# Performance work log

Hardware: AMD Instinct MI355X
Metric: run time of the kernel (lower is better)

The kernel has to match this reference:

```python
import jax, jax.numpy as jnp
import numpy as np
import math

B, S, D_MODEL, HEADS, GRID = 4, 2048, 512, 8, 8
HEAD_DIM = D_MODEL // HEADS
A_C, K_C, C_C = 0.9724108095811765, 0.9884401790754128, 0.999449553483052


def setup_inputs() -> dict:
    key = jax.random.key(0)
    ks = jax.random.split(key, 4)
    q = jax.random.normal(ks[0], (B, S, D_MODEL), jnp.float32)
    mask = jnp.tril(jnp.ones((S, S), dtype=bool))[None, None]  # causal (1,1,S,S)
    out_dim = 3 * D_MODEL
    grid_norm = jnp.arange(1, GRID + 1, dtype=jnp.float32)  # (grid,)
    # is_first=True init: normal(0,0.4)/output_dim/grid_norm_factor
    amplitudes = jax.random.normal(ks[1], (out_dim, D_MODEL, GRID), jnp.float32) * 0.4 / out_dim / grid_norm
    # norm_freq with is_first=True -> freq = arange(1..grid) / (grid+1)**0 = arange
    freq = jnp.arange(1, GRID + 1, dtype=jnp.float32)  # (grid,)
    grid_phase = jnp.arange(1, GRID + 1, dtype=jnp.float32) / (GRID + 1)
    input_phase = jnp.linspace(0.0, math.pi, D_MODEL, dtype=jnp.float32)[:, None]  # (in,1)
    phase0 = grid_phase[None, :] + input_phase  # (in, grid)
    ratio = 1.0
    for i in range(1, GRID):
        ratio *= A_C * i ** (-K_C) + C_C
    phase = phase0 * np.float32(ratio)
    kan_bias = jnp.ones((out_dim,), jnp.float32) / out_dim
    lim = math.sqrt(6.0 / (D_MODEL + D_MODEL))  # xavier_uniform
    out_w = jax.random.uniform(ks[2], (D_MODEL, D_MODEL), jnp.float32, -lim, lim)
    out_b = jnp.zeros((D_MODEL,), jnp.float32)
    return {"q": q, "mask": mask, "freq": freq, "phase": phase,
            "amplitudes": amplitudes, "kan_bias": kan_bias,
            "out_w": out_w, "out_b": out_b}


def sinekan(x2d, freq, phase, amp, bias):
    # y[n,j] = sum_{k,l} sin(x[n,k]*f[l] + p[k,l]) * amp[j,k,l] + bias[j]
    # expand sin(a+p) = sin(a)cos(p) + cos(a)sin(p); fold phase into weights
    ang = x2d[:, :, None] * freq  # (N, in, grid)
    w_sin = amp * jnp.cos(phase)  # (out, in, grid)
    w_cos = amp * jnp.sin(phase)
    y = (jnp.einsum('nkl,jkl->nj', jnp.sin(ang), w_sin)
         + jnp.einsum('nkl,jkl->nj', jnp.cos(ang), w_cos))
    return y + bias


def rotate_half(u):
    u1, u2 = jnp.split(u, 2, axis=-1)
    return jnp.concatenate([-u2, u1], axis=-1)


def apply_rope(x, pos_emb):
    cos, sin = jnp.split(pos_emb, 2, axis=-1)  # each (S, head_dim//2)
    x_even, x_odd = x[..., ::2], x[..., 1::2]
    x1 = x_even * cos + rotate_half(x_odd) * sin
    x2 = x_odd * cos + rotate_half(x_even) * sin
    return jnp.concatenate([x1, x2], axis=-1)


def rope_emb(seq_len, dim):
    half = dim // 2
    inv_freq = 1.0 / (10000.0 ** (jnp.arange(half, dtype=jnp.float32) / half))
    ang = jnp.arange(seq_len, dtype=jnp.float32)[:, None] * inv_freq  # (S, half)
    return jnp.concatenate([jnp.cos(ang), jnp.sin(ang)], axis=-1)  # (S, dim)


def reference(q, mask, freq, phase, amplitudes, kan_bias, out_w, out_b):
    b, s, _ = q.shape
    qkv = sinekan(q.reshape(-1, D_MODEL), freq, phase, amplitudes, kan_bias)
    qkv = qkv.reshape(b, s, HEADS, 3 * HEAD_DIM).transpose(0, 2, 1, 3)  # (b,h,s,3d)
    qs, ks, vs = jnp.split(qkv, 3, axis=-1)
    pe = rope_emb(s, HEAD_DIM)
    qs = apply_rope(qs, pe)
    ks = apply_rope(ks, pe)
    scores = jnp.einsum('bhqd,bhkd->bhqk', qs, ks) / math.sqrt(HEAD_DIM)
    scores = jnp.where(mask, scores.astype(jnp.float32), -1e9)
    attn = jax.nn.softmax(scores, axis=-1)
    ctx = jnp.einsum('bhqk,bhkd->bhqd', attn, vs)
    ctx = ctx.transpose(0, 2, 1, 3).reshape(b, s, D_MODEL)
    return ctx @ out_w.T + out_b
```

## Files before the change

kernel.cpp:

```cpp
#include <hip/hip_runtime.h>
#include <math.h>


typedef __attribute__((ext_vector_type(8))) short bf16x8;
typedef __attribute__((ext_vector_type(8))) unsigned short ushort8;
typedef __attribute__((ext_vector_type(4))) float f32x4;

#define DEV __device__ __forceinline__

DEV unsigned short f2bf(float f) {
  unsigned u = __builtin_bit_cast(unsigned, f);
  u += 0x7FFFu + ((u >> 16) & 1u);
  return (unsigned short)(u >> 16);
}
DEV float bf2f(unsigned short h) {
  unsigned u = ((unsigned)h) << 16;
  return __builtin_bit_cast(float, u);
}

#define GLDS16(gp, lp)                                                         \
  __builtin_amdgcn_global_load_lds(                                            \
      (const __attribute__((address_space(1))) void*)(gp),                     \
      (__attribute__((address_space(3))) void*)(lp), 16, 0, 0)

__global__ __launch_bounds__(256) void wprep(const float* __restrict__ amp,
                                             const float* __restrict__ phase,
                                             unsigned short* __restrict__ Wb) {
  int id = blockIdx.x * 256 + threadIdx.x;
  int j = id >> 9;
  int k = id & 511;
  const float* ap = amp + (size_t)id * 8;
  const float* ph = phase + k * 8;
  union { unsigned short u[16]; uint4 v[2]; } pk;
#pragma unroll
  for (int l = 0; l < 8; ++l) {
    float sp, cp;
    sincosf(ph[l], &sp, &cp);
    float a = ap[l];
    pk.u[l] = f2bf(a * cp);
    pk.u[8 + l] = f2bf(a * sp);
  }
  uint4* dst = (uint4*)(Wb + (size_t)j * 8192 + k * 16);
  dst[0] = pk.v[0];
  dst[1] = pk.v[1];
}

__global__ __launch_bounds__(256) void owprep(const float* __restrict__ w,
                                              unsigned short* __restrict__ o) {
  int id = blockIdx.x * 256 + threadIdx.x;
  o[id] = f2bf(w[id]);
}

__global__ __launch_bounds__(256) void fgen(const float* __restrict__ q,
                                            unsigned short* __restrict__ F) {
  int id = blockIdx.x * 256 + threadIdx.x;
  int row = id >> 9;
  int dim = id & 511;
  float x = q[(size_t)row * 512 + dim];
  float s1, c1;
  sincosf(x, &s1, &c1);
  union { unsigned short u[16]; uint4 v[2]; } fr;
  float s = s1, c = c1;
  fr.u[0] = f2bf(s);
  fr.u[8] = f2bf(c);
#pragma unroll
  for (int l = 1; l < 8; ++l) {
    float ns = s * c1 + c * s1;
    float nc = c * c1 - s * s1;
    s = ns; c = nc;
    fr.u[l] = f2bf(s);
    fr.u[8 + l] = f2bf(c);
  }
  uint4* dst = (uint4*)(F + (size_t)row * 8192 + dim * 16);
  dst[0] = fr.v[0];
  dst[1] = fr.v[1];
}

__global__ __launch_bounds__(512, 2) void kan_gemm8(
    const unsigned short* __restrict__ F, const unsigned short* __restrict__ Wb,
    const float* __restrict__ bias, unsigned short* __restrict__ qkv) {
  __shared__ __align__(16) char LDS[114688];

  const int tid = threadIdx.x, lane = tid & 63, wid = tid >> 6;
  const int wm = wid >> 2, wn = wid & 3;
  const int l15 = lane & 15, kg = lane >> 4;

  int bid = blockIdx.x;
  int xcd = bid & 7, u = bid >> 3;
  const int m0 = (xcd * 4 + (u & 3)) * 256;
  const int n0 = (u >> 2) * 192;

  const int growl = wid * 8 + (lane >> 3);
  const int cswz = ((lane & 7) ^ (lane >> 3)) << 4;

  f32x4 acc[2][4][3] = {};
  bf16x8 af0[4][2], af1[4][2], bf[3][2];

#define STAGE_A(T, C)                                                           \
  GLDS16((const char*)F + (size_t)(m0 + (C)*64 + growl) * 16384 +               \
             (size_t)(T) * 128 + cswz,                                          \
         LDS + (((T)&1) * 32768 + (C)*8192 + wid * 1024))

#define STAGE_B(T, C)                                                           \
  GLDS16((const char*)Wb + (size_t)(n0 + (C)*64 + growl) * 16384 +              \
             (size_t)(T) * 128 + cswz,                                          \
         LDS + (65536 + ((T)&1) * 24576 + (C)*8192 + wid * 1024))

#define DSREAD_A(DST, T, MQ)                                                    \
  do {                                                                          \
    _Pragma("unroll") for (int mi = 0; mi < 4; ++mi)                            \
        _Pragma("unroll") for (int kk = 0; kk < 2; ++kk) {                      \
      int _r = (MQ)*128 + wm * 64 + mi * 16 + l15;                              \
      DST[mi][kk] = *(const bf16x8*)(LDS + ((T)&1) * 32768 + _r * 128 +         \
                                     (((kk * 4 + kg) ^ (l15 & 7)) << 4));       \
    }                                                                           \
  } while (0)

#define DSREAD_B(T)                                                             \
  do {                                                                          \
    _Pragma("unroll") for (int ni = 0; ni < 3; ++ni)                            \
        _Pragma("unroll") for (int kk = 0; kk < 2; ++kk) {                      \
      int _r = wn * 48 + ni * 16 + l15;                                         \
      bf[ni][kk] = *(const bf16x8*)(LDS + 65536 + ((T)&1) * 24576 + _r * 128 +  \
                                    (((kk * 4 + kg) ^ (l15 & 7)) << 4));        \
    }                                                                           \
  } while (0)

#define MFMAS(AF, MQ, NI0, NI1)                                                 \
  do {                                                                          \
    __builtin_amdgcn_s_setprio(1);                                              \
    _Pragma("unroll") for (int mi = 0; mi < 4; ++mi)                            \
        _Pragma("unroll") for (int ni = (NI0); ni <= (NI1); ++ni)               \
            _Pragma("unroll") for (int kk = 0; kk < 2; ++kk)                    \
                acc[MQ][mi][ni] = __builtin_amdgcn_mfma_f32_16x16x32_bf16(      \
                    AF[mi][kk], bf[ni][kk], acc[MQ][mi][ni], 0, 0, 0);          \
    __builtin_amdgcn_s_setprio(0);                                              \
  } while (0)

#define BAR __builtin_amdgcn_s_barrier()
#define VMW(N) asm volatile("s_waitcnt vmcnt(" #N ")" ::: "memory")
#define LGW                                                                     \
  do {                                                                          \
    asm volatile("s_waitcnt lgkmcnt(0)" ::: "memory");                          \
    __builtin_amdgcn_sched_barrier(0);                                          \
  } while (0)

  STAGE_A(0, 0); STAGE_A(0, 1);
  STAGE_B(0, 0); STAGE_B(0, 1); STAGE_B(0, 2);
  STAGE_A(0, 2); STAGE_A(0, 3);

#pragma unroll 2
  for (int t = 0; t < 127; ++t) {
    VMW(2); BAR;
    DSREAD_A(af0, t, 0); DSREAD_B(t);
    STAGE_A(t + 1, 0); STAGE_A(t + 1, 1);
    LGW; MFMAS(af0, 0, 0, 1);
    BAR;
    DSREAD_A(af1, t, 1);
    STAGE_B(t + 1, 0); STAGE_B(t + 1, 1);
    MFMAS(af0, 0, 2, 2);
    VMW(4); BAR;
    STAGE_B(t + 1, 2); STAGE_A(t + 1, 2);
    MFMAS(af1, 1, 0, 1);
    BAR;
    STAGE_A(t + 1, 3);
    MFMAS(af1, 1, 2, 2);
  }
  {
    const int t = 127;
    VMW(2); BAR;
    DSREAD_A(af0, t, 0); DSREAD_B(t);
    LGW; MFMAS(af0, 0, 0, 1);
    BAR;
    DSREAD_A(af1, t, 1);
    MFMAS(af0, 0, 2, 2);
    VMW(0); BAR;
    MFMAS(af1, 1, 0, 1);
    BAR;
    MFMAS(af1, 1, 2, 2);
  }

#pragma unroll
  for (int mq = 0; mq < 2; ++mq)
#pragma unroll
    for (int mi = 0; mi < 4; ++mi)
#pragma unroll
      for (int ni = 0; ni < 3; ++ni) {
        int row = m0 + mq * 128 + wm * 64 + mi * 16 + kg * 4;
        int col = n0 + wn * 48 + ni * 16 + l15;
        float bv = bias[col];
        f32x4 a = acc[mq][mi][ni];
#pragma unroll
        for (int j = 0; j < 4; ++j)
          qkv[(size_t)(row + j) * 1536 + col] = f2bf(a[j] + bv);
      }
#undef STAGE_A
#undef STAGE_B
#undef DSREAD_A
#undef DSREAD_B
#undef MFMAS
#undef BAR
#undef VMW
#undef LGW
}

__global__ __launch_bounds__(256) void rope_prep(const unsigned short* __restrict__ qkv,
                                                 unsigned short* __restrict__ Qr,
                                                 unsigned short* __restrict__ Kr) {
  int id = blockIdx.x * 256 + threadIdx.x;
  int i = id & 31;
  int row = id >> 5;
  int s = row & 2047;
  int bh = row >> 11;
  int b = bh >> 3, h = bh & 7;

  const unsigned short* base = qkv + ((size_t)(b * 2048 + s)) * 1536 + h * 192;

  float inv = exp2f(-(float)i * (13.287712379549449f / 32.0f));
  float ang = (float)s * inv;
  float sn, cs;
  sincosf(ang, &sn, &cs);

  int pi = (i < 16) ? i + 16 : i - 16;
  float sign = (i < 16) ? -1.f : 1.f;
  size_t orow = (size_t)row * 64;

  {
    const unsigned short* xp = base;
    float xe = bf2f(xp[2 * i]), xo = bf2f(xp[2 * i + 1]);
    float po = bf2f(xp[2 * pi + 1]), pe = bf2f(xp[2 * pi]);
    Qr[orow + i] = f2bf(xe * cs + sign * po * sn);
    Qr[orow + 32 + i] = f2bf(xo * cs + sign * pe * sn);
  }
  {
    const unsigned short* xp = base + 64;
    float xe = bf2f(xp[2 * i]), xo = bf2f(xp[2 * i + 1]);
    float po = bf2f(xp[2 * pi + 1]), pe = bf2f(xp[2 * pi]);
    Kr[orow + i] = f2bf(xe * cs + sign * po * sn);
    Kr[orow + 32 + i] = f2bf(xo * cs + sign * pe * sn);
  }
}

__global__ __launch_bounds__(512) void attn(const unsigned short* __restrict__ Qr,
                                            const unsigned short* __restrict__ Kr,
                                            const unsigned short* __restrict__ qkv,
                                            unsigned short* __restrict__ ctx) {
  __shared__ __align__(16) char KB[8192];
  __shared__ __align__(16) char VT[8192];
  __shared__ __align__(16) char PL[18432];

  const int tid = threadIdx.x;
  const int lane = tid & 63;
  const int w = tid >> 6;
  const int qb = blockIdx.x;
  const int bh = blockIdx.y;
  const int b = bh >> 3, h = bh & 7;
  const int qw = qb * 128 + w * 16;
  const int l15 = lane & 15, kg = lane >> 4;

  const unsigned short* Qp = Qr + ((size_t)bh * 2048 + qw + l15) * 64 + kg * 8;
  bf16x8 qf0 = *(const bf16x8*)Qp;
  bf16x8 qf1 = *(const bf16x8*)(Qp + 32);

  f32x4 octx[4] = {};
  float den[4] = {0.f, 0.f, 0.f, 0.f};
  char* Pw = PL + w * 2304;

  const int skp = tid >> 3;
  const int sds = tid & 7;
  const int vd = tid & 63;
  const int vkq = tid >> 6;

  const int nkt = 2 * qb + 2;
  for (int kt = 0; kt < nkt; ++kt) {
    ushort8 kv =
        *(const ushort8*)(Kr + ((size_t)bh * 2048 + kt * 64 + skp) * 64 + sds * 8);
    *(ushort8*)(KB + ((skp * 128 + sds * 16) ^ ((skp & 7) << 4))) = kv;
    {
      const unsigned short* vcol =
          qkv + ((size_t)(b * 2048 + kt * 64 + vkq * 8)) * 1536 + h * 192 + 128 + vd;
      ushort8 vv;
#pragma unroll
      for (int jj = 0; jj < 8; ++jj) vv[jj] = vcol[jj * 1536];
      *(ushort8*)(VT + (vd * 128 + ((vkq * 16) ^ ((vd & 7) << 4)))) = vv;
    }
    __syncthreads();

    f32x4 zero = {0.f, 0.f, 0.f, 0.f};
#pragma unroll
    for (int f = 0; f < 4; ++f) {
      int kp = f * 16 + l15;
      int swk = (kp & 7) << 4;
      bf16x8 kf0 = *(const bf16x8*)(KB + ((kp * 128 + kg * 16) ^ swk));
      bf16x8 kf1 = *(const bf16x8*)(KB + ((kp * 128 + 64 + kg * 16) ^ swk));
      f32x4 sA = __builtin_amdgcn_mfma_f32_16x16x32_bf16(qf0, kf0, zero, 0, 0, 0);
      sA = __builtin_amdgcn_mfma_f32_16x16x32_bf16(qf1, kf1, sA, 0, 0, 0);
      int kgl = kt * 64 + kp;
#pragma unroll
      for (int j = 0; j < 4; ++j) {
        int qrow = qw + kg * 4 + j;
        float p = (kgl <= qrow) ? __expf(sA[j] * 0.125f) : 0.f;
        den[j] += p;
        int prow = kg * 4 + j;
        *(unsigned short*)(Pw + prow * 144 + kp * 2) = f2bf(p);
      }
    }
    bf16x8 pf0 = *(const bf16x8*)(Pw + l15 * 144 + kg * 16);
    bf16x8 pf1 = *(const bf16x8*)(Pw + l15 * 144 + 64 + kg * 16);
#pragma unroll
    for (int nd = 0; nd < 4; ++nd) {
      int d = nd * 16 + l15;
      int swv = (d & 7) << 4;
      bf16x8 vf0 = *(const bf16x8*)(VT + (d * 128 + ((kg * 16) ^ swv)));
      bf16x8 vf1 = *(const bf16x8*)(VT + (d * 128 + ((64 + kg * 16) ^ swv)));
      octx[nd] = __builtin_amdgcn_mfma_f32_16x16x32_bf16(pf0, vf0, octx[nd], 0, 0, 0);
      octx[nd] = __builtin_amdgcn_mfma_f32_16x16x32_bf16(pf1, vf1, octx[nd], 0, 0, 0);
    }
    __syncthreads();
  }

#pragma unroll
  for (int j = 0; j < 4; ++j) {
    float d_ = den[j];
    d_ += __shfl_xor(d_, 1);
    d_ += __shfl_xor(d_, 2);
    d_ += __shfl_xor(d_, 4);
    d_ += __shfl_xor(d_, 8);
    den[j] = d_;
  }
#pragma unroll
  for (int nd = 0; nd < 4; ++nd)
#pragma unroll
    for (int j = 0; j < 4; ++j) {
      int qrow = qw + kg * 4 + j;
      int col = h * 64 + nd * 16 + l15;
      ctx[((size_t)b * 2048 + qrow) * 512 + col] = f2bf(octx[nd][j] / den[j]);
    }
}

__global__ __launch_bounds__(256) void out_gemm(const unsigned short* __restrict__ A,
                                                const unsigned short* __restrict__ Bw,
                                                const float* __restrict__ outb,
                                                float* __restrict__ out) {
  __shared__ __align__(16) unsigned short Al[128 * 32];
  __shared__ __align__(16) unsigned short Bl[128 * 32];
  const int tid = threadIdx.x, lane = tid & 63, w = tid >> 6;
  const int wm = w >> 1, wn = w & 1;
  const int m0 = blockIdx.x * 128, n0 = blockIdx.y * 128;
  const int l15 = lane & 15, kg = lane >> 4;

  f32x4 acc[4][4] = {};

  const unsigned short* ga = A + (size_t)(m0 + (tid >> 2)) * 512 + (tid & 3) * 8;
  const unsigned short* gb = Bw + (size_t)(n0 + (tid >> 2)) * 512 + (tid & 3) * 8;

  for (int t = 0; t < 16; ++t) {
    GLDS16(ga + t * 32, &Al[w * 512]);
    GLDS16(ga + t * 32 + 64 * 512, &Al[2048 + w * 512]);
    GLDS16(gb + t * 32, &Bl[w * 512]);
    GLDS16(gb + t * 32 + 64 * 512, &Bl[2048 + w * 512]);
    __syncthreads();

    bf16x8 af[4], bfr[4];
#pragma unroll
    for (int m = 0; m < 4; ++m)
      af[m] = *(const bf16x8*)&Al[(wm * 64 + m * 16 + l15) * 32 + kg * 8];
#pragma unroll
    for (int n = 0; n < 4; ++n)
      bfr[n] = *(const bf16x8*)&Bl[(wn * 64 + n * 16 + l15) * 32 + kg * 8];
#pragma unroll
    for (int m = 0; m < 4; ++m)
#pragma unroll
      for (int n = 0; n < 4; ++n)
        acc[m][n] =
            __builtin_amdgcn_mfma_f32_16x16x32_bf16(af[m], bfr[n], acc[m][n], 0, 0, 0);

    __syncthreads();
  }

  const int rb = m0 + wm * 64 + kg * 4;
  const int cb = n0 + wn * 64 + l15;
#pragma unroll
  for (int n = 0; n < 4; ++n) {
    int cc = cb + n * 16;
    float bv = outb[cc];
#pragma unroll
    for (int m = 0; m < 4; ++m)
#pragma unroll
      for (int j = 0; j < 4; ++j)
        out[(size_t)(rb + m * 16 + j) * 512 + cc] = acc[m][n][j] + bv;
  }
}

extern "C" void kernel_launch(void* const* d_in, const int* in_sizes, int n_in,
                              void* d_out, int out_size, void* d_ws, size_t ws_size,
                              hipStream_t stream) {
  const float* q = (const float*)d_in[0];
  const float* phase = (const float*)d_in[3];
  const float* amp = (const float*)d_in[4];
  const float* kbias = (const float*)d_in[5];
  const float* out_w = (const float*)d_in[6];
  const float* out_b = (const float*)d_in[7];
  float* out = (float*)d_out;

  char* p = (char*)d_ws;
  unsigned short* Wb = (unsigned short*)(p);
  unsigned short* qkv = (unsigned short*)(p + 25165824);
  unsigned short* Qr = (unsigned short*)(p + 50331648);
  unsigned short* Kr = (unsigned short*)(p + 58720256);
  unsigned short* ctx = (unsigned short*)(p + 67108864);
  unsigned short* Wob = (unsigned short*)(p + 75497472);
  unsigned short* F = (unsigned short*)(p + 76021760);

  owprep<<<1024, 256, 0, stream>>>(out_w, Wob);
  wprep<<<3072, 256, 0, stream>>>(amp, phase, Wb);
  fgen<<<16384, 256, 0, stream>>>(q, F);
  kan_gemm8<<<256, 512, 0, stream>>>(F, Wb, kbias, qkv);
  rope_prep<<<8192, 256, 0, stream>>>(qkv, Qr, Kr);
  attn<<<dim3(16, 32), 512, 0, stream>>>(Qr, Kr, qkv, ctx);
  out_gemm<<<dim3(64, 4), 256, 0, stream>>>(ctx, Wob, out_b, out);
}
```

Baseline: 303.2 us.

## Pair low and high causal query tiles per attention block for load balance

Each attention block now handles two 64-row query tiles, one from the start and one from the end of the sequence, so every block processes 33 key tiles instead of a count that grows with block index. Blocks shrink to 256 threads, and each K/V tile loaded into shared memory is reused by both query tiles. This removes the causal tail imbalance where late blocks did far more work than early ones. In exchange each wave holds twice the accumulators, which raises register pressure, and there are fewer waves per block to hide latency.

```diff
diff --git a/kernel.cpp b/kernel.cpp
--- a/kernel.cpp
+++ b/kernel.cpp
@@ -241,29 +241,33 @@
   }
 }
 
-__global__ __launch_bounds__(512) void attn(const unsigned short* __restrict__ Qr,
+__global__ __launch_bounds__(256) void attn(const unsigned short* __restrict__ Qr,
                                             const unsigned short* __restrict__ Kr,
                                             const unsigned short* __restrict__ qkv,
                                             unsigned short* __restrict__ ctx) {
   __shared__ __align__(16) char KB[8192];
   __shared__ __align__(16) char VT[8192];
-  __shared__ __align__(16) char PL[18432];
+  __shared__ __align__(16) char PL[9216];
 
   const int tid = threadIdx.x;
   const int lane = tid & 63;
   const int w = tid >> 6;
-  const int qb = blockIdx.x;
+  const int qp = blockIdx.x;
   const int bh = blockIdx.y;
   const int b = bh >> 3, h = bh & 7;
-  const int qw = qb * 128 + w * 16;
+  const int qwL = qp * 64 + w * 16;
+  const int qwH = (31 - qp) * 64 + w * 16;
   const int l15 = lane & 15, kg = lane >> 4;
 
-  const unsigned short* Qp = Qr + ((size_t)bh * 2048 + qw + l15) * 64 + kg * 8;
-  bf16x8 qf0 = *(const bf16x8*)Qp;
-  bf16x8 qf1 = *(const bf16x8*)(Qp + 32);
-
-  f32x4 octx[4] = {};
-  float den[4] = {0.f, 0.f, 0.f, 0.f};
+  const unsigned short* QpL = Qr + ((size_t)bh * 2048 + qwL + l15) * 64 + kg * 8;
+  const unsigned short* QpH = Qr + ((size_t)bh * 2048 + qwH + l15) * 64 + kg * 8;
+  bf16x8 qfL0 = *(const bf16x8*)QpL;
+  bf16x8 qfL1 = *(const bf16x8*)(QpL + 32);
+  bf16x8 qfH0 = *(const bf16x8*)QpH;
+  bf16x8 qfH1 = *(const bf16x8*)(QpH + 32);
+
+  f32x4 octxL[4] = {}, octxH[4] = {};
+  float denL[4] = {0.f, 0.f, 0.f, 0.f}, denH[4] = {0.f, 0.f, 0.f, 0.f};
   char* Pw = PL + w * 2304;
 
   const int skp = tid >> 3;
@@ -271,70 +275,84 @@
   const int vd = tid & 63;
   const int vkq = tid >> 6;
 
-  const int nkt = 2 * qb + 2;
-  for (int kt = 0; kt < nkt; ++kt) {
-    ushort8 kv =
-        *(const ushort8*)(Kr + ((size_t)bh * 2048 + kt * 64 + skp) * 64 + sds * 8);
-    *(ushort8*)(KB + ((skp * 128 + sds * 16) ^ ((skp & 7) << 4))) = kv;
-    {
+#define QKPV(QF0, QF1, OCTX, DEN, QW)                                          \
+  do {                                                                         \
+    f32x4 zero = {0.f, 0.f, 0.f, 0.f};                                         \
+    _Pragma("unroll") for (int f = 0; f < 4; ++f) {                            \
+      int kp = f * 16 + l15;                                                   \
+      int swk = (kp & 7) << 4;                                                 \
+      bf16x8 kf0 = *(const bf16x8*)(KB + ((kp * 128 + kg * 16) ^ swk));        \
+      bf16x8 kf1 = *(const bf16x8*)(KB + ((kp * 128 + 64 + kg * 16) ^ swk));   \
+      f32x4 sA =                                                               \
+          __builtin_amdgcn_mfma_f32_16x16x32_bf16(QF0, kf0, zero, 0, 0, 0);    \
+      sA = __builtin_amdgcn_mfma_f32_16x16x32_bf16(QF1, kf1, sA, 0, 0, 0);     \
+      int kgl = kt * 64 + kp;                                                  \
+      _Pragma("unroll") for (int j = 0; j < 4; ++j) {                          \
+        int qrow = (QW) + kg * 4 + j;                                          \
+        float pp = (kgl <= qrow) ? __expf(sA[j] * 0.125f) : 0.f;               \
+        DEN[j] += pp;                                                          \
+        int prow = kg * 4 + j;                                                 \
+        *(unsigned short*)(Pw + prow * 144 + kp * 2) = f2bf(pp);               \
+      }                                                                        \
+    }                                                                          \
+    bf16x8 pf0 = *(const bf16x8*)(Pw + l15 * 144 + kg * 16);                   \
+    bf16x8 pf1 = *(const bf16x8*)(Pw + l15 * 144 + 64 + kg * 16);              \
+    _Pragma("unroll") for (int nd = 0; nd < 4; ++nd) {                         \
+      int d = nd * 16 + l15;                                                   \
+      int swv = (d & 7) << 4;                                                  \
+      bf16x8 vf0 = *(const bf16x8*)(VT + (d * 128 + ((kg * 16) ^ swv)));       \
+      bf16x8 vf1 = *(const bf16x8*)(VT + (d * 128 + ((64 + kg * 16) ^ swv)));  \
+      OCTX[nd] =                                                               \
+          __builtin_amdgcn_mfma_f32_16x16x32_bf16(pf0, vf0, OCTX[nd], 0, 0, 0);\
+      OCTX[nd] =                                                               \
+          __builtin_amdgcn_mfma_f32_16x16x32_bf16(pf1, vf1, OCTX[nd], 0, 0, 0);\
+    }                                                                          \
+  } while (0)
+
+  const int nktH = 32 - qp;
+  const int nktL = qp + 1;
+  for (int kt = 0; kt < nktH; ++kt) {
+#pragma unroll
+    for (int r = 0; r < 2; ++r) {
+      int krow = r * 32 + skp;
+      ushort8 kv = *(const ushort8*)(Kr + ((size_t)bh * 2048 + kt * 64 + krow) * 64 +
+                                     sds * 8);
+      *(ushort8*)(KB + ((krow * 128 + sds * 16) ^ ((krow & 7) << 4))) = kv;
       const unsigned short* vcol =
-          qkv + ((size_t)(b * 2048 + kt * 64 + vkq * 8)) * 1536 + h * 192 + 128 + vd;
+          qkv + ((size_t)(b * 2048 + kt * 64 + r * 32 + vkq * 8)) * 1536 +
+          h * 192 + 128 + vd;
       ushort8 vv;
 #pragma unroll
       for (int jj = 0; jj < 8; ++jj) vv[jj] = vcol[jj * 1536];
-      *(ushort8*)(VT + (vd * 128 + ((vkq * 16) ^ ((vd & 7) << 4)))) = vv;
+      int slot = r * 4 + vkq;
+      *(ushort8*)(VT + (vd * 128 + ((slot * 16) ^ ((vd & 7) << 4)))) = vv;
     }
     __syncthreads();
 
-    f32x4 zero = {0.f, 0.f, 0.f, 0.f};
-#pragma unroll
-    for (int f = 0; f < 4; ++f) {
-      int kp = f * 16 + l15;
-      int swk = (kp & 7) << 4;
-      bf16x8 kf0 = *(const bf16x8*)(KB + ((kp * 128 + kg * 16) ^ swk));
-      bf16x8 kf1 = *(const bf16x8*)(KB + ((kp * 128 + 64 + kg * 16) ^ swk));
-      f32x4 sA = __builtin_amdgcn_mfma_f32_16x16x32_bf16(qf0, kf0, zero, 0, 0, 0);
-      sA = __builtin_amdgcn_mfma_f32_16x16x32_bf16(qf1, kf1, sA, 0, 0, 0);
-      int kgl = kt * 64 + kp;
-#pragma unroll
-      for (int j = 0; j < 4; ++j) {
-        int qrow = qw + kg * 4 + j;
-        float p = (kgl <= qrow) ? __expf(sA[j] * 0.125f) : 0.f;
-        den[j] += p;
-        int prow = kg * 4 + j;
-        *(unsigned short*)(Pw + prow * 144 + kp * 2) = f2bf(p);
-      }
-    }
-    bf16x8 pf0 = *(const bf16x8*)(Pw + l15 * 144 + kg * 16);
-    bf16x8 pf1 = *(const bf16x8*)(Pw + l15 * 144 + 64 + kg * 16);
-#pragma unroll
-    for (int nd = 0; nd < 4; ++nd) {
-      int d = nd * 16 + l15;
-      int swv = (d & 7) << 4;
-      bf16x8 vf0 = *(const bf16x8*)(VT + (d * 128 + ((kg * 16) ^ swv)));
-      bf16x8 vf1 = *(const bf16x8*)(VT + (d * 128 + ((64 + kg * 16) ^ swv)));
-      octx[nd] = __builtin_amdgcn_mfma_f32_16x16x32_bf16(pf0, vf0, octx[nd], 0, 0, 0);
-      octx[nd] = __builtin_amdgcn_mfma_f32_16x16x32_bf16(pf1, vf1, octx[nd], 0, 0, 0);
-    }
+    QKPV(qfH0, qfH1, octxH, denH, qwH);
+    if (kt < nktL) QKPV(qfL0, qfL1, octxL, denL, qwL);
     __syncthreads();
   }
+#undef QKPV
 
 #pragma unroll
   for (int j = 0; j < 4; ++j) {
-    float d_ = den[j];
-    d_ += __shfl_xor(d_, 1);
-    d_ += __shfl_xor(d_, 2);
-    d_ += __shfl_xor(d_, 4);
-    d_ += __shfl_xor(d_, 8);
-    den[j] = d_;
+    float dH = denH[j], dL = denL[j];
+    dH += __shfl_xor(dH, 1); dL += __shfl_xor(dL, 1);
+    dH += __shfl_xor(dH, 2); dL += __shfl_xor(dL, 2);
+    dH += __shfl_xor(dH, 4); dL += __shfl_xor(dL, 4);
+    dH += __shfl_xor(dH, 8); dL += __shfl_xor(dL, 8);
+    denH[j] = dH; denL[j] = dL;
   }
 #pragma unroll
   for (int nd = 0; nd < 4; ++nd)
 #pragma unroll
     for (int j = 0; j < 4; ++j) {
-      int qrow = qw + kg * 4 + j;
       int col = h * 64 + nd * 16 + l15;
-      ctx[((size_t)b * 2048 + qrow) * 512 + col] = f2bf(octx[nd][j] / den[j]);
+      int qrowH = qwH + kg * 4 + j;
+      int qrowL = qwL + kg * 4 + j;
+      ctx[((size_t)b * 2048 + qrowH) * 512 + col] = f2bf(octxH[nd][j] / denH[j]);
+      ctx[((size_t)b * 2048 + qrowL) * 512 + col] = f2bf(octxL[nd][j] / denL[j]);
     }
 }
 
@@ -417,6 +435,6 @@
   fgen<<<16384, 256, 0, stream>>>(q, F);
   kan_gemm8<<<256, 512, 0, stream>>>(F, Wb, kbias, qkv);
   rope_prep<<<8192, 256, 0, stream>>>(qkv, Qr, Kr);
-  attn<<<dim3(16, 32), 512, 0, stream>>>(Qr, Kr, qkv, ctx);
+  attn<<<dim3(16, 32), 256, 0, stream>>>(Qr, Kr, qkv, ctx);
   out_gemm<<<dim3(64, 4), 256, 0, stream>>>(ctx, Wob, out_b, out);
 }
```

Measured after the change: 289.2 us, median of 2. 1.05x faster.
